# Kernel optimization log

Measured on AMD Instinct MI355X. Metric: run time of the kernel, lower is better.

The kernel has to match this reference:

```python
import jax, jax.numpy as jnp
import numpy as np

D = 3            # input_ch (pos dims)
L = 16           # n_levels
F = 2            # n_feats per level
LOG2 = 19
CAP = 1 << LOG2  # hashmap capacity per level
COARSEST, FINEST = 16.0, 2048.0
N = 524288
D1 = D + 1
HASH_MULT = np.int32(2531011)


def _elevate_matrix():
    # Linear map R^D -> hyperplane {sum=0} in R^{D+1} (Adams et al. permutohedral lattice)
    sf = 1.0 / np.sqrt(np.arange(1, D + 1, dtype=np.float64) * np.arange(2, D + 2, dtype=np.float64))
    E = np.zeros((D1, D), np.float32)
    E[0, :] = sf
    for i in range(1, D1):
        E[i, i - 1] = -i * sf[i - 1]
        E[i, i:] = sf[i:]
    return E


def _scales():
    g = (FINEST / COARSEST) ** (np.arange(L, dtype=np.float64) / (L - 1))
    return (COARSEST * g).astype(np.float32)


def permuto_forward(pos, params):
    E = jnp.asarray(_elevate_matrix())
    scales = jnp.asarray(_scales())
    x = pos[None] * scales[:, None, None]              # [L,N,D]
    elev = jnp.einsum('vp,lnp->lnv', E, x)             # [L,N,D1]
    # nearest lattice remainder-0 point (multiples of D1)
    rem0f = jnp.round(elev / D1) * D1
    sums = (jnp.sum(rem0f, -1) / D1).astype(jnp.int32)  # exactly integer
    di = elev - rem0f
    # rank[i] = #{j : d_j > d_i  or (d_j == d_i and j < i)}
    gt = di[..., None, :] > di[..., :, None]
    eq = di[..., None, :] == di[..., :, None]
    jlt = jnp.arange(D1)[None, :] < jnp.arange(D1)[:, None]
    rank = jnp.sum(gt | (eq & jlt), -1).astype(jnp.int32) + sums[..., None]
    rem0 = rem0f.astype(jnp.int32)
    under = (rank < 0).astype(jnp.int32)
    over = (rank > D).astype(jnp.int32)
    rank = rank + (under - over) * D1
    rem0 = rem0 + (under - over) * D1
    # barycentric weights of the D1 simplex vertices
    delta = (elev - rem0.astype(elev.dtype)) / D1      # [L,N,D1]
    dbr = jnp.take_along_axis(delta, jnp.argsort(rank, -1), -1)  # delta ordered by rank
    w0 = 1.0 + dbr[..., -1] - dbr[..., 0]
    w = jnp.concatenate([w0[..., None], -(dbr[..., 1:] - dbr[..., :-1])[..., ::-1]], -1)  # [L,N,D1]
    # integer keys of the D1 simplex vertices (first D coords; last is implicit)
    kk = jnp.arange(D1, dtype=jnp.int32)
    keys = (rem0[..., None, :D] + kk[:, None]
            - D1 * (rank[..., None, :D] > (D - kk[:, None])).astype(jnp.int32))  # [L,N,D1,D]
    # hash: k = (k + key_i) * 2531011, wrap in 32 bits, mask to capacity (pow2)
    h = jnp.zeros(keys.shape[:-1], jnp.int32)
    for i in range(D):
        h = (h + keys[..., i]) * HASH_MULT
    idx = h & (CAP - 1)                                # [L,N,D1]
    flat_idx = idx + jnp.arange(L, dtype=jnp.int32)[:, None, None] * CAP
    feats = params.reshape(L * CAP, F)[flat_idx]       # [L,N,D1,F]
    out = jnp.einsum('lnv,lnvf->lnf', w, feats)        # [L,N,F]
    return jnp.moveaxis(out, 0, 1).reshape(pos.shape[0], L * F)


def setup_inputs() -> dict:
    key = jax.random.key(0)
    k1, k2 = jax.random.split(key)
    pos = jax.random.uniform(k1, (N, D), jnp.float32)                 # coords in [0,1)
    params = jax.random.normal(k2, (L * CAP * F,), jnp.float32) * 1e-4  # param_init std
    return {"input": pos, "flattened_params": params}


def reference(input, flattened_params):
    return permuto_forward(input, flattened_params)
```

## Files before the change

### kernel.cpp

```cpp
#include <hip/hip_runtime.h>
#include <hip/hip_fp16.h>
#include <cmath>

namespace {

typedef float    vf4 __attribute__((ext_vector_type(4)));
typedef unsigned uv2 __attribute__((ext_vector_type(2)));

constexpr int kN = 524288;
constexpr int kL = 16;
constexpr int kCapLog2 = 19;
constexpr int kCap = 1 << kCapLog2;
constexpr int kCapMask = kCap - 1;
constexpr unsigned kHashMult = 2531011u;

constexpr int kHalf = kN / 2;
constexpr int kHB   = kHalf / 256;
constexpr int kPB   = kN / 256;

constexpr int cD[4][3]   = {{ 8, 8, 6},{10,10, 9},{13,12,10},{17,16,14}};
constexpr int cB[4][3]   = {{-4,-16,-16},{-4,-20,-24},{-4,-24,-28},{-4,-32,-40}};
constexpr int cOff[4]    = {0, 1536, 5136, 11376};
constexpr int kDenseCnt  = 26608;

constexpr int kMegaMain  = 15360;
constexpr int kBuildBlks = 104;
constexpr int kConvBaseF4 = 7 * (kCap * 2 / 4);

struct ScaleArr { float s[kL]; };

__device__ __forceinline__ void permuto_point(
    float x0, float x1, float x2, int rem0[4], int rank[4], float w[4])
{
    const float E00 = (float)( 0.70710678118654752440);
    const float E01 = (float)( 0.40824829046386301637);
    const float E02 = (float)( 0.28867513459481288225);
    const float E10 = (float)(-0.70710678118654752440);
    const float E21 = (float)(-2.0 * 0.40824829046386301637);
    const float E32 = (float)(-3.0 * 0.28867513459481288225);

    float elev[4];
    elev[0] = E00 * x0 + E01 * x1 + E02 * x2;
    elev[1] = E10 * x0 + E01 * x1 + E02 * x2;
    elev[2] =            E21 * x1 + E02 * x2;
    elev[3] =                       E32 * x2;

    float rem0f[4], di[4];
    #pragma unroll
    for (int v = 0; v < 4; ++v) {
        rem0f[v] = rintf(elev[v] * 0.25f) * 4.0f;
        di[v]    = elev[v] - rem0f[v];
    }
    const int sums = (int)((((rem0f[0] + rem0f[1]) + rem0f[2]) + rem0f[3]) * 0.25f);

    #pragma unroll
    for (int a = 0; a < 4; ++a) {
        int r = 0;
        #pragma unroll
        for (int b = 0; b < 4; ++b)
            r += (di[b] > di[a]) || (di[b] == di[a] && b < a);
        rank[a] = r + sums;
        rem0[a] = (int)rem0f[a];
    }
    #pragma unroll
    for (int v = 0; v < 4; ++v) {
        if (rank[v] < 0)      { rank[v] += 4; rem0[v] += 4; }
        else if (rank[v] > 3) { rank[v] -= 4; rem0[v] -= 4; }
    }

    float dbr[4];
    #pragma unroll
    for (int v = 0; v < 4; ++v)
        dbr[rank[v] & 3] = (elev[v] - (float)rem0[v]) * 0.25f;

    w[0] = (1.0f + dbr[3]) - dbr[0];
    w[1] = dbr[2] - dbr[3];
    w[2] = dbr[1] - dbr[2];
    w[3] = dbr[0] - dbr[1];
}

__device__ __forceinline__ void fine_job(
    const float* __restrict__ pos, const unsigned* __restrict__ tab,
    unsigned* __restrict__ out_t16, const ScaleArr& sc, int level, int n)
{
    const float s  = sc.s[level];
    const float x0 = __builtin_nontemporal_load(pos + 3 * n + 0) * s;
    const float x1 = __builtin_nontemporal_load(pos + 3 * n + 1) * s;
    const float x2 = __builtin_nontemporal_load(pos + 3 * n + 2) * s;

    int rem0[4], rank[4];
    float w[4];
    permuto_point(x0, x1, x2, rem0, rank, w);

    const unsigned* __restrict__ t = tab + ((size_t)level << kCapLog2);
    int hidx[4];
    #pragma unroll
    for (int k = 0; k < 4; ++k) {
        int h = 0;
        #pragma unroll
        for (int i = 0; i < 3; ++i) {
            const int key = rem0[i] + k - 4 * (rank[i] > 3 - k);
            h = (int)((unsigned)(h + key) * kHashMult);
        }
        hidx[k] = h & kCapMask;
    }
    unsigned e[4];
    #pragma unroll
    for (int k = 0; k < 4; ++k) e[k] = t[hidx[k]];

    float o0 = 0.0f, o1 = 0.0f;
    #pragma unroll
    for (int k = 0; k < 4; ++k) {
        const __half2 hv = *reinterpret_cast<const __half2*>(&e[k]);
        o0 += w[k] * __low2float(hv);
        o1 += w[k] * __high2float(hv);
    }
    const __half2 po = __floats2half2_rn(o0, o1);
    __builtin_nontemporal_store(*reinterpret_cast<const unsigned*>(&po),
                                out_t16 + ((size_t)level << kCapLog2) + n);
}

__device__ __forceinline__ void coarse_job(
    const float* __restrict__ pos, const unsigned* __restrict__ dense,
    unsigned* __restrict__ out_t16, const ScaleArr& sc, int n)
{
    const float p0 = __builtin_nontemporal_load(pos + 3 * n + 0);
    const float p1 = __builtin_nontemporal_load(pos + 3 * n + 1);
    const float p2 = __builtin_nontemporal_load(pos + 3 * n + 2);

    #pragma unroll 1
    for (int l = 0; l < 4; ++l) {
        const float s = sc.s[l];
        int rem0[4], rank[4];
        float w[4];
        permuto_point(p0 * s, p1 * s, p2 * s, rem0, rank, w);

        const unsigned* __restrict__ dl = dense + cOff[l];
        unsigned ev[4];
        #pragma unroll
        for (int k = 0; k < 4; ++k) {
            const int i0 = (rem0[0] - 4 * (rank[0] > 3 - k) - cB[l][0]) >> 2;
            const int i1 = (rem0[1] - 4 * (rank[1] > 3 - k) - cB[l][1]) >> 2;
            const int i2 = (rem0[2] - 4 * (rank[2] > 3 - k) - cB[l][2]) >> 2;
            ev[k] = dl[((k * cD[l][0] + i0) * cD[l][1] + i1) * cD[l][2] + i2];
        }
        float o0 = 0.0f, o1 = 0.0f;
        #pragma unroll
        for (int k = 0; k < 4; ++k) {
            const __half2 hv = *reinterpret_cast<const __half2*>(&ev[k]);
            o0 += w[k] * __low2float(hv);
            o1 += w[k] * __high2float(hv);
        }
        const __half2 po = __floats2half2_rn(o0, o1);
        __builtin_nontemporal_store(*reinterpret_cast<const unsigned*>(&po),
                                    out_t16 + ((size_t)l << kCapLog2) + n);
    }
}

__device__ __forceinline__ void transpose_job(
    const unsigned* __restrict__ out_t16, vf4* __restrict__ out4,
    int pb, unsigned (*tile)[17])
{
    const int t  = threadIdx.x;
    const int p0 = pb * 256;

    #pragma unroll
    for (int l = 0; l < kL; ++l)
        tile[t][l] = __builtin_nontemporal_load(out_t16 + ((size_t)l << kCapLog2) + p0 + t);
    __syncthreads();

    const size_t base = (size_t)p0 * 8;
    #pragma unroll
    for (int j = 0; j < 4; ++j) {
        const int idx = j * 256 + t;
        const int p = idx >> 2, q = idx & 3;
        float f[8];
        #pragma unroll
        for (int i = 0; i < 4; ++i) {
            const unsigned u = tile[p][4 * q + i];
            const __half2 hv = *reinterpret_cast<const __half2*>(&u);
            f[2 * i + 0] = __low2float(hv);
            f[2 * i + 1] = __high2float(hv);
        }
        vf4 a, c;
        a.x = f[0]; a.y = f[1]; a.z = f[2]; a.w = f[3];
        c.x = f[4]; c.y = f[5]; c.z = f[6]; c.w = f[7];
        out4[base + (size_t)p * 8 + 2 * q + 0] = a;
        out4[base + (size_t)p * 8 + 2 * q + 1] = c;
    }
}

__global__ __launch_bounds__(256) void mega1(
    const float* __restrict__ pos,
    const float* __restrict__ params,
    unsigned* __restrict__ tab,
    unsigned* __restrict__ out_t16,
    unsigned* __restrict__ dense,
    ScaleArr sc)
{
    const int b = blockIdx.x;
    if (b < kMegaMain) {
        const int q = b / 5, r = b % 5;
        if (r < 2) {
            const int idx   = q * 2 + r;
            const int level = 4 + (idx >> 11);
            const int n     = ((idx & 2047) << 8) + threadIdx.x;

            const float s  = sc.s[level];
            const float x0 = __builtin_nontemporal_load(pos + 3 * n + 0) * s;
            const float x1 = __builtin_nontemporal_load(pos + 3 * n + 1) * s;
            const float x2 = __builtin_nontemporal_load(pos + 3 * n + 2) * s;

            int rem0[4], rank[4];
            float w[4];
            permuto_point(x0, x1, x2, rem0, rank, w);

            const float2* __restrict__ t2 =
                (const float2*)params + ((size_t)level << kCapLog2);
            int hidx[4];
            #pragma unroll
            for (int k = 0; k < 4; ++k) {
                int h = 0;
                #pragma unroll
                for (int i = 0; i < 3; ++i) {
                    const int key = rem0[i] + k - 4 * (rank[i] > 3 - k);
                    h = (int)((unsigned)(h + key) * kHashMult);
                }
                hidx[k] = h & kCapMask;
            }
            float2 f[4];
            #pragma unroll
            for (int k = 0; k < 4; ++k) f[k] = t2[hidx[k]];

            float o0 = 0.0f, o1 = 0.0f;
            #pragma unroll
            for (int k = 0; k < 4; ++k) { o0 += w[k] * f[k].x; o1 += w[k] * f[k].y; }

            const __half2 po = __floats2half2_rn(o0, o1);
            __builtin_nontemporal_store(*reinterpret_cast<const unsigned*>(&po),
                                        out_t16 + ((size_t)level << kCapLog2) + n);
        } else {
            const int i  = q * 3 + (r - 2);
            const int jj = kConvBaseF4 + i * 256 + threadIdx.x;
            vf4 v = __builtin_nontemporal_load((const vf4*)params + jj);
            __half2 a = __floats2half2_rn(v.x, v.y);
            __half2 c = __floats2half2_rn(v.z, v.w);
            uv2 o;
            o.x = *reinterpret_cast<unsigned*>(&a);
            o.y = *reinterpret_cast<unsigned*>(&c);
            __builtin_nontemporal_store(o, (uv2*)tab + jj);
        }
    } else {
        const int e = (b - kMegaMain) * 256 + threadIdx.x;
        if (e >= kDenseCnt) return;
        int l, r;
        if      (e < cOff[1]) { l = 0; r = e; }
        else if (e < cOff[2]) { l = 1; r = e - cOff[1]; }
        else if (e < cOff[3]) { l = 2; r = e - cOff[2]; }
        else                  { l = 3; r = e - cOff[3]; }
        const int d0 = cD[l][0], d1 = cD[l][1], d2 = cD[l][2];
        const int per = d0 * d1 * d2;
        int rr = r;
        const int k  = rr / per;  rr -= k * per;
        const int i0 = rr / (d1 * d2); rr -= i0 * (d1 * d2);
        const int i1 = rr / d2;
        const int i2 = rr - i1 * d2;

        const int key0 = cB[l][0] + 4 * i0 + k;
        const int key1 = cB[l][1] + 4 * i1 + k;
        const int key2 = cB[l][2] + 4 * i2 + k;
        int h = 0;
        h = (int)((unsigned)(h + key0) * kHashMult);
        h = (int)((unsigned)(h + key1) * kHashMult);
        h = (int)((unsigned)(h + key2) * kHashMult);
        const size_t entry = ((size_t)l << kCapLog2) + (h & kCapMask);
        const __half2 hv = __floats2half2_rn(params[entry * 2], params[entry * 2 + 1]);
        dense[e] = *reinterpret_cast<const unsigned*>(&hv);
    }
}

__global__ __launch_bounds__(256, 8) void gatherA(
    const float* __restrict__ pos,
    const unsigned* __restrict__ tab,
    const unsigned* __restrict__ dense,
    unsigned* __restrict__ out_t16,
    ScaleArr sc)
{
    const int b = blockIdx.x;
    if (b < 8 * kHB) {
        const int level = 7 + (b & 7);
        const int n = ((b >> 3) << 8) + threadIdx.x;
        fine_job(pos, tab, out_t16, sc, level, n);
    } else if (b < 9 * kHB) {
        const int q = b - 8 * kHB;
        const int c = (q >> 3) + ((q & 7) << 7);
        const int n = (c << 8) + threadIdx.x;
        fine_job(pos, tab, out_t16, sc, 15, n);
    } else {
        coarse_job(pos, dense, out_t16, sc, (b - 9 * kHB) * 256 + threadIdx.x);
    }
}

__global__ __launch_bounds__(256, 8) void gatherB(
    const float* __restrict__ pos,
    const unsigned* __restrict__ tab,
    const unsigned* __restrict__ out_t16c,
    unsigned* __restrict__ out_t16,
    vf4* __restrict__ out4,
    ScaleArr sc)
{
    __shared__ unsigned tile[256][17];
    const int b = blockIdx.x;
    if (b < 8 * kHB) {
        const int level = 7 + (b & 7);
        const int n = kHalf + ((b >> 3) << 8) + threadIdx.x;
        fine_job(pos, tab, out_t16, sc, level, n);
    } else if (b < 9 * kHB) {
        const int q = b - 8 * kHB;
        const int c = (q >> 3) + ((q & 7) << 7);
        const int n = kHalf + (c << 8) + threadIdx.x;
        fine_job(pos, tab, out_t16, sc, 15, n);
    } else {
        transpose_job(out_t16c, out4, b - 9 * kHB, tile);
    }
}

__global__ __launch_bounds__(256) void transposeB(
    const unsigned* __restrict__ out_t16, vf4* __restrict__ out4)
{
    __shared__ unsigned tile[256][17];
    transpose_job(out_t16, out4, blockIdx.x + kHB, tile);
}

__global__ __launch_bounds__(256) void permuto_fwd(
    const float* __restrict__ pos,
    const float* __restrict__ params,
    float* __restrict__ out,
    ScaleArr sc)
{
    const int gid = blockIdx.x * 256 + threadIdx.x;
    const int l = gid & (kL - 1);
    const int n = gid >> 4;

    const float s  = sc.s[l];
    const float x0 = pos[3 * n + 0] * s;
    const float x1 = pos[3 * n + 1] * s;
    const float x2 = pos[3 * n + 2] * s;

    int rem0[4], rank[4];
    float w[4];
    permuto_point(x0, x1, x2, rem0, rank, w);

    const float2* __restrict__ tab = (const float2*)params + ((size_t)l << kCapLog2);
    float o0 = 0.0f, o1 = 0.0f;
    #pragma unroll
    for (int k = 0; k < 4; ++k) {
        int h = 0;
        #pragma unroll
        for (int i = 0; i < 3; ++i) {
            const int key = rem0[i] + k - 4 * (rank[i] > 3 - k);
            h = (int)((unsigned)(h + key) * kHashMult);
        }
        const float2 f = tab[h & kCapMask];
        o0 += w[k] * f.x;
        o1 += w[k] * f.y;
    }
    ((float2*)out)[(n << 4) + l] = make_float2(o0, o1);
}

}

extern "C" void kernel_launch(void* const* d_in, const int* in_sizes, int n_in,
                              void* d_out, int out_size, void* d_ws, size_t ws_size,
                              hipStream_t stream) {
    const float* pos    = (const float*)d_in[0];
    const float* params = (const float*)d_in[1];
    float* out          = (float*)d_out;

    ScaleArr sc;
    for (int l = 0; l < kL; ++l)
        sc.s[l] = (float)(16.0 * pow(128.0, (double)l / 15.0));

    const size_t tab_bytes   = (size_t)kL * kCap * 4;
    const size_t outt_bytes  = (size_t)kL * kN * 4;
    const size_t dense_bytes = (size_t)kDenseCnt * 4;

    if (ws_size >= tab_bytes + outt_bytes + dense_bytes) {
        unsigned* tab     = (unsigned*)d_ws;
        unsigned* out_t16 = (unsigned*)((char*)d_ws + tab_bytes);
        unsigned* dense   = (unsigned*)((char*)d_ws + tab_bytes + outt_bytes);

        mega1<<<kMegaMain + kBuildBlks, 256, 0, stream>>>(pos, params, tab, out_t16, dense, sc);
        gatherA<<<9 * kHB + kPB, 256, 0, stream>>>(pos, tab, dense, out_t16, sc);
        gatherB<<<9 * kHB + kHB, 256, 0, stream>>>(pos, tab, out_t16, out_t16, (vf4*)out, sc);
        transposeB<<<kHB, 256, 0, stream>>>(out_t16, (vf4*)out);
    } else {
        permuto_fwd<<<(kN * kL) / 256, 256, 0, stream>>>(pos, params, out, sc);
    }
}
```

Measured before the change: 171.5 us.

## Split fine-level gathers into three point chunks, overlapping each transpose with the next gather

The fine-level gather work is split into three point ranges instead of two, each handled by its own kernel. Each later kernel transposes the previous chunk's output while gathering its own chunk, and the coarse job now runs first in gatherA. The level-15 block remapping that strided chunks across points is replaced with a linear order. The goal is a smaller non-overlapped tail transpose and better overlap of transpose with gather, at the cost of one more kernel launch and a possible change in cache locality for level 15.

```diff
diff --git a/kernel.cpp b/kernel.cpp
--- a/kernel.cpp
+++ b/kernel.cpp
@@ -14,9 +14,9 @@
 constexpr int kCapMask = kCap - 1;
 constexpr unsigned kHashMult = 2531011u;
 
-constexpr int kHalf = kN / 2;
-constexpr int kHB   = kHalf / 256;
-constexpr int kPB   = kN / 256;
+constexpr int kPB  = kN / 256;
+constexpr int kT0 = 682, kT1 = 682, kT2 = 684;
+constexpr int kOffA = 0, kOffB = kT0, kOffC = kT0 + kT1;
 
 constexpr int cD[4][3]   = {{ 8, 8, 6},{10,10, 9},{13,12,10},{17,16,14}};
 constexpr int cB[4][3]   = {{-4,-16,-16},{-4,-20,-24},{-4,-24,-28},{-4,-32,-40}};
@@ -287,49 +287,71 @@
     ScaleArr sc)
 {
     const int b = blockIdx.x;
-    if (b < 8 * kHB) {
-        const int level = 7 + (b & 7);
-        const int n = ((b >> 3) << 8) + threadIdx.x;
+    if (b < kPB) {
+        coarse_job(pos, dense, out_t16, sc, b * 256 + threadIdx.x);
+    } else if (b < kPB + 8 * kT0) {
+        const int q = b - kPB;
+        const int level = 7 + (q & 7);
+        const int n = ((kOffA + (q >> 3)) << 8) + threadIdx.x;
         fine_job(pos, tab, out_t16, sc, level, n);
-    } else if (b < 9 * kHB) {
-        const int q = b - 8 * kHB;
-        const int c = (q >> 3) + ((q & 7) << 7);
-        const int n = (c << 8) + threadIdx.x;
+    } else {
+        const int q = b - kPB - 8 * kT0;
+        const int n = ((kOffA + q) << 8) + threadIdx.x;
         fine_job(pos, tab, out_t16, sc, 15, n);
-    } else {
-        coarse_job(pos, dense, out_t16, sc, (b - 9 * kHB) * 256 + threadIdx.x);
     }
 }
 
 __global__ __launch_bounds__(256, 8) void gatherB(
     const float* __restrict__ pos,
     const unsigned* __restrict__ tab,
-    const unsigned* __restrict__ out_t16c,
     unsigned* __restrict__ out_t16,
     vf4* __restrict__ out4,
     ScaleArr sc)
 {
     __shared__ unsigned tile[256][17];
     const int b = blockIdx.x;
-    if (b < 8 * kHB) {
-        const int level = 7 + (b & 7);
-        const int n = kHalf + ((b >> 3) << 8) + threadIdx.x;
+    if (b < kT0) {
+        transpose_job(out_t16, out4, kOffA + b, tile);
+    } else if (b < kT0 + 8 * kT1) {
+        const int q = b - kT0;
+        const int level = 7 + (q & 7);
+        const int n = ((kOffB + (q >> 3)) << 8) + threadIdx.x;
         fine_job(pos, tab, out_t16, sc, level, n);
-    } else if (b < 9 * kHB) {
-        const int q = b - 8 * kHB;
-        const int c = (q >> 3) + ((q & 7) << 7);
-        const int n = kHalf + (c << 8) + threadIdx.x;
+    } else {
+        const int q = b - kT0 - 8 * kT1;
+        const int n = ((kOffB + q) << 8) + threadIdx.x;
         fine_job(pos, tab, out_t16, sc, 15, n);
+    }
+}
+
+__global__ __launch_bounds__(256, 8) void gatherC(
+    const float* __restrict__ pos,
+    const unsigned* __restrict__ tab,
+    unsigned* __restrict__ out_t16,
+    vf4* __restrict__ out4,
+    ScaleArr sc)
+{
+    __shared__ unsigned tile[256][17];
+    const int b = blockIdx.x;
+    if (b < kT1) {
+        transpose_job(out_t16, out4, kOffB + b, tile);
+    } else if (b < kT1 + 8 * kT2) {
+        const int q = b - kT1;
+        const int level = 7 + (q & 7);
+        const int n = ((kOffC + (q >> 3)) << 8) + threadIdx.x;
+        fine_job(pos, tab, out_t16, sc, level, n);
     } else {
-        transpose_job(out_t16c, out4, b - 9 * kHB, tile);
-    }
-}
-
-__global__ __launch_bounds__(256) void transposeB(
+        const int q = b - kT1 - 8 * kT2;
+        const int n = ((kOffC + q) << 8) + threadIdx.x;
+        fine_job(pos, tab, out_t16, sc, 15, n);
+    }
+}
+
+__global__ __launch_bounds__(256) void transposeC(
     const unsigned* __restrict__ out_t16, vf4* __restrict__ out4)
 {
     __shared__ unsigned tile[256][17];
-    transpose_job(out_t16, out4, blockIdx.x + kHB, tile);
+    transpose_job(out_t16, out4, kOffC + blockIdx.x, tile);
 }
 
 __global__ __launch_bounds__(256) void permuto_fwd(
@@ -391,9 +413,10 @@
         unsigned* dense   = (unsigned*)((char*)d_ws + tab_bytes + outt_bytes);
 
         mega1<<<kMegaMain + kBuildBlks, 256, 0, stream>>>(pos, params, tab, out_t16, dense, sc);
-        gatherA<<<9 * kHB + kPB, 256, 0, stream>>>(pos, tab, dense, out_t16, sc);
-        gatherB<<<9 * kHB + kHB, 256, 0, stream>>>(pos, tab, out_t16, out_t16, (vf4*)out, sc);
-        transposeB<<<kHB, 256, 0, stream>>>(out_t16, (vf4*)out);
+        gatherA<<<kPB + 9 * kT0, 256, 0, stream>>>(pos, tab, dense, out_t16, sc);
+        gatherB<<<kT0 + 9 * kT1, 256, 0, stream>>>(pos, tab, out_t16, (vf4*)out, sc);
+        gatherC<<<kT1 + 9 * kT2, 256, 0, stream>>>(pos, tab, out_t16, (vf4*)out, sc);
+        transposeC<<<kT2, 256, 0, stream>>>(out_t16, (vf4*)out);
     } else {
         permuto_fwd<<<(kN * kL) / 256, 256, 0, stream>>>(pos, params, out, sc);
     }
```

New measurement: 174.2 us. Within noise of the previous version (+1.6%).
